# Kernel optimization log

Measured on AMD Instinct MI355X. Metric: run time of the kernel, lower is better.

The kernel has to match this reference:

```python
import jax, jax.numpy as jnp
import numpy as np

B, S, E, H = 2, 2048, 1024, 16
HD = E // H
CLAMP = 5.0


def setup_inputs() -> dict:
    key = jax.random.key(0)
    k1, k2, k3, k4 = jax.random.split(key, 4)
    # xavier-uniform-ish scale for weights
    lim_qkv = float(np.sqrt(6.0 / (E + 3 * E)))
    lim_o = float(np.sqrt(6.0 / (E + E)))
    return {
        "x": jax.random.normal(k1, (B, S, E), dtype=jnp.float32),
        "attn_bias": jax.random.normal(k2, (B, H, S, S), dtype=jnp.float32),
        "Wqkv": jax.random.uniform(k3, (3 * E, E), dtype=jnp.float32, minval=-lim_qkv, maxval=lim_qkv),
        "bqkv": jnp.zeros((3 * E,), dtype=jnp.float32),
        "Wo": jax.random.uniform(k4, (E, E), dtype=jnp.float32, minval=-lim_o, maxval=lim_o),
        "bo": jnp.zeros((E,), dtype=jnp.float32),
    }


def reference(x, attn_bias, Wqkv, bqkv, Wo, bo):
    b, s, e = x.shape
    # QKV projection: [B,S,3E] -> [B,S,H,3*HD] -> [B,H,S,3*HD]
    qkv = jnp.einsum("bse,fe->bsf", x, Wqkv) + bqkv
    qkv = qkv.reshape(b, s, H, 3 * HD).transpose(0, 2, 1, 3)
    q, k, v = jnp.split(qkv, 3, axis=-1)  # each [B,H,S,HD]
    # logits: bias added BEFORE 1/sqrt(d_k) scaling (as in source)
    logits = jnp.einsum("bhqd,bhkd->bhqk", q, k)
    logits = (logits + attn_bias) / jnp.sqrt(jnp.float32(HD))
    logits = jnp.clip(logits, -CLAMP, CLAMP)
    attn = jax.nn.softmax(logits, axis=-1)
    vals = jnp.einsum("bhqk,bhkd->bhqd", attn, v)
    vals = vals.transpose(0, 2, 1, 3).reshape(b, s, e)
    return jnp.einsum("bse,fe->bsf", vals, Wo) + bo
```

## Files before the change

kernel.cpp:

```cpp
#include <hip/hip_runtime.h>
#include <hip/hip_bf16.h>

#define NB 2
#define NS 2048
#define NE 1024
#define NH 16
#define HD 64

typedef __hip_bfloat16 bf16;
typedef __attribute__((ext_vector_type(8))) short bf16x8;
typedef __attribute__((ext_vector_type(4))) float f32x4;

typedef __attribute__((address_space(3))) void* lds_p;
typedef const __attribute__((address_space(1))) void* glb_p;

#define MFMA16(a, b, c) __builtin_amdgcn_mfma_f32_16x16x32_bf16((a), (b), (c), 0, 0, 0)

__device__ __forceinline__ void gl_lds16(const void* g, void* l) {
    __builtin_amdgcn_global_load_lds((glb_p)g, (lds_p)l, 16, 0, 0);
}

__device__ __forceinline__ bf16x8 ldv8(const bf16* p) { return *(const bf16x8*)p; }

__global__ __launch_bounds__(256) void cast3_k(const float* __restrict__ x,
                                               const float* __restrict__ wqkv,
                                               const float* __restrict__ wo,
                                               bf16* __restrict__ xb,
                                               bf16* __restrict__ wqkvb,
                                               bf16* __restrict__ wob) {
    const int n_x = NB * NS * NE / 4;
    const int n_q = 3 * NE * NE / 4;
    const int n_o = NE * NE / 4;
    int i = blockIdx.x * 256 + threadIdx.x;
    const float* in;
    bf16* out;
    int j;
    if (i < n_x) {
        in = x; out = xb; j = i;
    } else if (i < n_x + n_q) {
        in = wqkv; out = wqkvb; j = i - n_x;
    } else if (i < n_x + n_q + n_o) {
        in = wo; out = wob; j = i - n_x - n_q;
    } else {
        return;
    }
    float4 v = ((const float4*)in)[j];
    union { ushort4 u; bf16 b[4]; } pk;
    pk.b[0] = __float2bfloat16(v.x);
    pk.b[1] = __float2bfloat16(v.y);
    pk.b[2] = __float2bfloat16(v.z);
    pk.b[3] = __float2bfloat16(v.w);
    ((ushort4*)out)[j] = pk.u;
}

__global__ __launch_bounds__(256) void qkv_gemm(const bf16* __restrict__ A,
                                                const bf16* __restrict__ Bm,
                                                const float* __restrict__ bqkv,
                                                bf16* __restrict__ Qb, bf16* __restrict__ Kb,
                                                bf16* __restrict__ Vtb) {
    __shared__ bf16 As[128 * 32];
    __shared__ bf16 Bs[128 * 32];
    const int brow = blockIdx.x * 128;
    const int bcol = blockIdx.y * 128;
    const int t = threadIdx.x;
    const int w = t >> 6, lane = t & 63;
    const int wr = (w >> 1) * 64, wc = (w & 1) * 64;
    const int lr = lane & 15, lh = lane >> 4;
    const int K = 1024;

    f32x4 acc[4][4];
#pragma unroll
    for (int m = 0; m < 4; ++m)
#pragma unroll
        for (int n = 0; n < 4; ++n) acc[m][n] = (f32x4){0.f, 0.f, 0.f, 0.f};

    const bf16* ga0 = A + (size_t)(brow + (t >> 2)) * K + (t & 3) * 8;
    const bf16* ga1 = A + (size_t)(brow + 64 + (t >> 2)) * K + (t & 3) * 8;
    const bf16* gb0 = Bm + (size_t)(bcol + (t >> 2)) * K + (t & 3) * 8;
    const bf16* gb1 = Bm + (size_t)(bcol + 64 + (t >> 2)) * K + (t & 3) * 8;
    bf16* la0 = As + t * 8;
    bf16* la1 = As + 2048 + t * 8;
    bf16* lb0 = Bs + t * 8;
    bf16* lb1 = Bs + 2048 + t * 8;

    for (int kt = 0; kt < K; kt += 32) {
        gl_lds16(ga0 + kt, la0);
        gl_lds16(ga1 + kt, la1);
        gl_lds16(gb0 + kt, lb0);
        gl_lds16(gb1 + kt, lb1);
        __syncthreads();
        bf16x8 af[4], bfv[4];
#pragma unroll
        for (int m = 0; m < 4; ++m) af[m] = ldv8(&As[(wr + m * 16 + lr) * 32 + lh * 8]);
#pragma unroll
        for (int n = 0; n < 4; ++n) bfv[n] = ldv8(&Bs[(wc + n * 16 + lr) * 32 + lh * 8]);
#pragma unroll
        for (int m = 0; m < 4; ++m)
#pragma unroll
            for (int n = 0; n < 4; ++n) acc[m][n] = MFMA16(af[m], bfv[n], acc[m][n]);
        __syncthreads();
    }

#pragma unroll
    for (int n = 0; n < 4; ++n) {
        const int col = bcol + wc + n * 16 + lr;
        const int h = col / 192;
        const int r = col - h * 192;
        const int wh = r >> 6;
        const int d = r & 63;
        const float bq = bqkv[col];
#pragma unroll
        for (int m = 0; m < 4; ++m) {
            const int row0 = brow + wr + m * 16 + lh * 4;
            const int b = row0 >> 11;
            const int s0 = row0 & 2047;
            const size_t hb = (size_t)(b * NH + h) * (NS * HD);
            if (wh == 2) {
                alignas(8) bf16 tmp[4];
#pragma unroll
                for (int i = 0; i < 4; ++i) tmp[i] = __float2bfloat16(acc[m][n][i] + bq);
                *(ushort4*)(Vtb + hb + (size_t)d * NS + s0) = *(const ushort4*)tmp;
            } else {
                bf16* dst = (wh == 0 ? Qb : Kb) + hb + (size_t)s0 * HD + d;
#pragma unroll
                for (int i = 0; i < 4; ++i) dst[(size_t)i * HD] = __float2bfloat16(acc[m][n][i] + bq);
            }
        }
    }
}

__global__ __launch_bounds__(256, 4) void attn_k(const bf16* __restrict__ Qb,
                                                 const bf16* __restrict__ Kb,
                                                 const bf16* __restrict__ Vtb,
                                                 const float* __restrict__ bias,
                                                 bf16* __restrict__ valsb) {
    const int L = blockIdx.x;
    const int xcd = L & 7, kk = L >> 3;
    const int bh = (xcd << 2) | (kk >> 5);
    const int q0 = (kk & 31) * 64;
    const int t = threadIdx.x;
    const int w = t >> 6, lane = t & 63;
    const int lr = lane & 15, lh = lane >> 4;

    __shared__ bf16 Kls[2][64 * 64];
    __shared__ bf16 Vls[2][64 * 64];
    __shared__ bf16 Ps[4][16 * 64];

    const bf16* Qp = Qb + (size_t)bh * NS * HD;
    const bf16* Kp = Kb + (size_t)bh * NS * HD;
    const bf16* Vp = Vtb + (size_t)bh * HD * NS;

    const int qw = q0 + w * 16;
    bf16x8 qf0 = ldv8(&Qp[(qw + lr) * HD + lh * 8]);
    bf16x8 qf1 = ldv8(&Qp[(qw + lr) * HD + 32 + lh * 8]);

    const float* Bp = bias + (size_t)bh * NS * NS + (size_t)(qw + lr) * NS + lh * 4;

    const int srow0 = t >> 3;
    const int sce0 = ((t & 7) * 8) ^ ((srow0 & 7) << 3);
    const int srow1 = srow0 + 32;
    const int sce1 = ((t & 7) * 8) ^ ((srow1 & 7) << 3);

    f32x4 acc_o[4];
    float rowsum = 0.f;
#pragma unroll
    for (int n = 0; n < 4; ++n) acc_o[n] = (f32x4){0.f, 0.f, 0.f, 0.f};

    const float C1 = 0.18033688011112042f;
    const float C2 = 7.2134752044448170f;

    const int rswz = (lr & 7) << 3;
    const int ce0 = (lh * 8) ^ rswz;
    const int ce1 = (32 + lh * 8) ^ rswz;
    const int pswz = (lr & 7) << 3;

    gl_lds16(Kp + (size_t)srow0 * HD + sce0, &Kls[0][t * 8]);
    gl_lds16(Kp + (size_t)srow1 * HD + sce1, &Kls[0][2048 + t * 8]);
    gl_lds16(Vp + (size_t)srow0 * NS + sce0, &Vls[0][t * 8]);
    gl_lds16(Vp + (size_t)srow1 * NS + sce1, &Vls[0][2048 + t * 8]);
    __builtin_amdgcn_sched_barrier(0);
    float4 bvA[4], bvB[4];
#pragma unroll
    for (int n = 0; n < 4; ++n) bvA[n] = *(const float4*)(Bp + n * 16);
    __builtin_amdgcn_sched_barrier(0);
#pragma unroll
    for (int n = 0; n < 4; ++n) bvB[n] = *(const float4*)(Bp + 64 + n * 16);
    __builtin_amdgcn_sched_barrier(0);
    asm volatile("s_waitcnt vmcnt(8)" ::: "memory");
    __builtin_amdgcn_sched_barrier(0);
    __builtin_amdgcn_s_barrier();
    __builtin_amdgcn_sched_barrier(0);

#define ATTN_COMPUTE(CUR, BV)                                                         \
    {                                                                                 \
        const bf16* Kc = &Kls[CUR][0];                                                \
        f32x4 s[4];                                                                   \
        _Pragma("unroll") for (int n = 0; n < 4; ++n) {                               \
            bf16x8 k0 = ldv8(&Kc[(n * 16 + lr) * 64 + ce0]);                          \
            bf16x8 k1 = ldv8(&Kc[(n * 16 + lr) * 64 + ce1]);                          \
            s[n] = (f32x4){0.f, 0.f, 0.f, 0.f};                                       \
            s[n] = MFMA16(k0, qf0, s[n]);                                             \
            s[n] = MFMA16(k1, qf1, s[n]);                                             \
        }                                                                             \
        _Pragma("unroll") for (int n = 0; n < 4; ++n) {                               \
            union { ushort4 u; bf16 b[4]; } pk;                                       \
            _Pragma("unroll") for (int i = 0; i < 4; ++i) {                           \
                float bb = (i == 0   ? BV[n].x                                        \
                            : i == 1 ? BV[n].y                                        \
                            : i == 2 ? BV[n].z                                        \
                                     : BV[n].w);                                      \
                float xv = (s[n][i] + bb) * C1;                                       \
                xv = fminf(fmaxf(xv, -C2), C2);                                       \
                float p = exp2f(xv);                                                  \
                rowsum += p;                                                          \
                pk.b[i] = __float2bfloat16(p);                                        \
            }                                                                         \
            *(ushort4*)&Ps[w][lr * 64 + ((n * 16 + lh * 4) ^ pswz)] = pk.u;           \
        }                                                                             \
        bf16x8 pa0 = ldv8(&Ps[w][lr * 64 + ((lh * 8) ^ pswz)]);                       \
        bf16x8 pa1 = ldv8(&Ps[w][lr * 64 + (((32 + lh * 8)) ^ pswz)]);                \
        const bf16* Vc = &Vls[CUR][0];                                                \
        _Pragma("unroll") for (int n = 0; n < 4; ++n) {                               \
            bf16x8 v0 = ldv8(&Vc[(n * 16 + lr) * 64 + ce0]);                          \
            bf16x8 v1 = ldv8(&Vc[(n * 16 + lr) * 64 + ce1]);                          \
            acc_o[n] = MFMA16(pa0, v0, acc_o[n]);                                     \
            acc_o[n] = MFMA16(pa1, v1, acc_o[n]);                                     \
        }                                                                             \
    }

#define TILESTEP(CUR, BV, KTN)                                                        \
    {                                                                                 \
        bf16* Kd = &Kls[(CUR) ^ 1][0];                                                \
        bf16* Vd = &Vls[(CUR) ^ 1][0];                                                \
        gl_lds16(Kp + (size_t)((KTN) + srow0) * HD + sce0, Kd + t * 8);               \
        gl_lds16(Kp + (size_t)((KTN) + srow1) * HD + sce1, Kd + 2048 + t * 8);        \
        gl_lds16(Vp + (size_t)srow0 * NS + (KTN) + sce0, Vd + t * 8);                 \
        gl_lds16(Vp + (size_t)srow1 * NS + (KTN) + sce1, Vd + 2048 + t * 8);          \
        __builtin_amdgcn_sched_barrier(0);                                            \
        ATTN_COMPUTE(CUR, BV)                                                         \
        __builtin_amdgcn_sched_barrier(0);                                            \
        _Pragma("unroll") for (int n = 0; n < 4; ++n)                                 \
            BV[n] = *(const float4*)(Bp + (KTN) + 64 + n * 16);                       \
        __builtin_amdgcn_sched_barrier(0);                                            \
        asm volatile("s_waitcnt vmcnt(4)" ::: "memory");                              \
        __builtin_amdgcn_sched_barrier(0);                                            \
        __builtin_amdgcn_s_barrier();                                                 \
        __builtin_amdgcn_sched_barrier(0);                                            \
    }

    for (int it = 0; it < 15; ++it) {
        const int tt = it * 2;
        TILESTEP(0, bvA, (tt + 1) * 64)
        TILESTEP(1, bvB, (tt + 2) * 64)
    }

    {
        const int ktn = 31 * 64;
        bf16* Kd = &Kls[1][0];
        bf16* Vd = &Vls[1][0];
        gl_lds16(Kp + (size_t)(ktn + srow0) * HD + sce0, Kd + t * 8);
        gl_lds16(Kp + (size_t)(ktn + srow1) * HD + sce1, Kd + 2048 + t * 8);
        gl_lds16(Vp + (size_t)srow0 * NS + ktn + sce0, Vd + t * 8);
        gl_lds16(Vp + (size_t)srow1 * NS + ktn + sce1, Vd + 2048 + t * 8);
        __builtin_amdgcn_sched_barrier(0);
        ATTN_COMPUTE(0, bvA)
        __builtin_amdgcn_sched_barrier(0);
        asm volatile("s_waitcnt vmcnt(0)" ::: "memory");
        __builtin_amdgcn_sched_barrier(0);
        __builtin_amdgcn_s_barrier();
        __builtin_amdgcn_sched_barrier(0);
    }
    ATTN_COMPUTE(1, bvB)
#undef TILESTEP
#undef ATTN_COMPUTE

    rowsum += __shfl_xor(rowsum, 16, 64);
    rowsum += __shfl_xor(rowsum, 32, 64);
    float inv[4];
#pragma unroll
    for (int i = 0; i < 4; ++i) inv[i] = 1.0f / __shfl(rowsum, lh * 4 + i, 64);

    const int b = bh >> 4, h = bh & 15;
#pragma unroll
    for (int n = 0; n < 4; ++n) {
#pragma unroll
        for (int i = 0; i < 4; ++i) {
            const int qrow = qw + lh * 4 + i;
            valsb[(size_t)(b * NS + qrow) * NE + h * HD + n * 16 + lr] =
                __float2bfloat16(acc_o[n][i] * inv[i]);
        }
    }
}

__global__ __launch_bounds__(256) void out_gemm(const bf16* __restrict__ A,
                                                const bf16* __restrict__ Bm,
                                                const float* __restrict__ bo,
                                                float* __restrict__ out) {
    __shared__ bf16 As[128 * 32];
    __shared__ bf16 Bs[64 * 32];
    const int brow = blockIdx.x * 128;
    const int bcol = blockIdx.y * 64;
    const int t = threadIdx.x;
    const int w = t >> 6, lane = t & 63;
    const int wr = (w >> 1) * 64, wc = (w & 1) * 32;
    const int lr = lane & 15, lh = lane >> 4;
    const int K = 1024;

    f32x4 acc[4][2];
#pragma unroll
    for (int m = 0; m < 4; ++m)
#pragma unroll
        for (int n = 0; n < 2; ++n) acc[m][n] = (f32x4){0.f, 0.f, 0.f, 0.f};

    const bf16* ga0 = A + (size_t)(brow + (t >> 2)) * K + (t & 3) * 8;
    const bf16* ga1 = A + (size_t)(brow + 64 + (t >> 2)) * K + (t & 3) * 8;
    const bf16* gb0 = Bm + (size_t)(bcol + (t >> 2)) * K + (t & 3) * 8;
    bf16* la0 = As + t * 8;
    bf16* la1 = As + 2048 + t * 8;
    bf16* lb0 = Bs + t * 8;

    for (int kt = 0; kt < K; kt += 32) {
        gl_lds16(ga0 + kt, la0);
        gl_lds16(ga1 + kt, la1);
        gl_lds16(gb0 + kt, lb0);
        __syncthreads();
        bf16x8 af[4], bfv[2];
#pragma unroll
        for (int m = 0; m < 4; ++m) af[m] = ldv8(&As[(wr + m * 16 + lr) * 32 + lh * 8]);
#pragma unroll
        for (int n = 0; n < 2; ++n) bfv[n] = ldv8(&Bs[(wc + n * 16 + lr) * 32 + lh * 8]);
#pragma unroll
        for (int m = 0; m < 4; ++m)
#pragma unroll
            for (int n = 0; n < 2; ++n) acc[m][n] = MFMA16(af[m], bfv[n], acc[m][n]);
        __syncthreads();
    }

#pragma unroll
    for (int n = 0; n < 2; ++n) {
        const int col = bcol + wc + n * 16 + lr;
        const float bv = bo[col];
#pragma unroll
        for (int m = 0; m < 4; ++m) {
            const int row0 = brow + wr + m * 16 + lh * 4;
#pragma unroll
            for (int i = 0; i < 4; ++i) out[(size_t)(row0 + i) * NE + col] = acc[m][n][i] + bv;
        }
    }
}

extern "C" void kernel_launch(void* const* d_in, const int* in_sizes, int n_in,
                              void* d_out, int out_size, void* d_ws, size_t ws_size,
                              hipStream_t stream) {
    const float* x = (const float*)d_in[0];
    const float* attn_bias = (const float*)d_in[1];
    const float* Wqkv = (const float*)d_in[2];
    const float* bqkv = (const float*)d_in[3];
    const float* Wo = (const float*)d_in[4];
    const float* bo = (const float*)d_in[5];
    float* out = (float*)d_out;

    char* ws = (char*)d_ws;
    bf16* xb = (bf16*)(ws);
    bf16* Wqkvb = (bf16*)(ws + (8u << 20));
    bf16* Wob = (bf16*)(ws + (14u << 20));
    bf16* Qb = (bf16*)(ws + (16u << 20));
    bf16* Kb = (bf16*)(ws + (24u << 20));
    bf16* Vtb = (bf16*)(ws + (32u << 20));
    bf16* valsb = (bf16*)(ws + (40u << 20));

    cast3_k<<<8192, 256, 0, stream>>>(x, Wqkv, Wo, xb, Wqkvb, Wob);

    qkv_gemm<<<dim3(32, 24), 256, 0, stream>>>(xb, Wqkvb, bqkv, Qb, Kb, Vtb);

    attn_k<<<dim3(1024), 256, 0, stream>>>(Qb, Kb, Vtb, attn_bias, valsb);

    out_gemm<<<dim3(32, 16), 256, 0, stream>>>(valsb, Wob, bo, out);
}
```

Measured before the change: 212.0 us.

## Double-buffer GEMM LDS tiles, XCD-aware block mapping, prefetch bias earlier in attention

Both GEMMs now use two LDS buffers, so the next K-tile's global-to-LDS load is issued before the current tile is computed. The QKV GEMM also flattens its grid and remaps block indices so that blocks landing on the same XCD share column tiles, aiming for better L2 reuse of weights. The attention loop adds a third bias register set and issues the bias load for the next tile before the compute instead of after it, to hide global latency. This costs more LDS and registers, and the double-buffered GEMM loop has no wait on the async LDS loads before the barrier, which may be a correctness risk.

After: 230.1 us. 8.5% more time.

```diff
diff --git a/kernel.cpp b/kernel.cpp
--- a/kernel.cpp
+++ b/kernel.cpp
@@ -58,10 +58,12 @@
                                                 const float* __restrict__ bqkv,
                                                 bf16* __restrict__ Qb, bf16* __restrict__ Kb,
                                                 bf16* __restrict__ Vtb) {
-    __shared__ bf16 As[128 * 32];
-    __shared__ bf16 Bs[128 * 32];
-    const int brow = blockIdx.x * 128;
-    const int bcol = blockIdx.y * 128;
+    __shared__ bf16 As[2][128 * 32];
+    __shared__ bf16 Bs[2][128 * 32];
+    const int L = blockIdx.x;
+    const int xcd = L & 7, j = L >> 3;
+    const int bcol = (xcd * 3 + j % 3) * 128;
+    const int brow = (j / 3) * 128;
     const int t = threadIdx.x;
     const int w = t >> 6, lane = t & 63;
     const int wr = (w >> 1) * 64, wc = (w & 1) * 64;
@@ -78,28 +80,34 @@
     const bf16* ga1 = A + (size_t)(brow + 64 + (t >> 2)) * K + (t & 3) * 8;
     const bf16* gb0 = Bm + (size_t)(bcol + (t >> 2)) * K + (t & 3) * 8;
     const bf16* gb1 = Bm + (size_t)(bcol + 64 + (t >> 2)) * K + (t & 3) * 8;
-    bf16* la0 = As + t * 8;
-    bf16* la1 = As + 2048 + t * 8;
-    bf16* lb0 = Bs + t * 8;
-    bf16* lb1 = Bs + 2048 + t * 8;
-
-    for (int kt = 0; kt < K; kt += 32) {
-        gl_lds16(ga0 + kt, la0);
-        gl_lds16(ga1 + kt, la1);
-        gl_lds16(gb0 + kt, lb0);
-        gl_lds16(gb1 + kt, lb1);
-        __syncthreads();
+
+#define QKV_STAGE(S, B)                                                   \
+    {                                                                     \
+        gl_lds16(ga0 + (S) * 32, &As[B][0] + t * 8);                      \
+        gl_lds16(ga1 + (S) * 32, &As[B][2048] + t * 8);                   \
+        gl_lds16(gb0 + (S) * 32, &Bs[B][0] + t * 8);                      \
+        gl_lds16(gb1 + (S) * 32, &Bs[B][2048] + t * 8);                   \
+    }
+
+    QKV_STAGE(0, 0)
+    __syncthreads();
+
+    for (int tt = 0; tt < 32; ++tt) {
+        if (tt + 1 < 32) QKV_STAGE(tt + 1, (tt + 1) & 1)
+        const bf16* Ab = &As[tt & 1][0];
+        const bf16* Bb = &Bs[tt & 1][0];
         bf16x8 af[4], bfv[4];
 #pragma unroll
-        for (int m = 0; m < 4; ++m) af[m] = ldv8(&As[(wr + m * 16 + lr) * 32 + lh * 8]);
-#pragma unroll
-        for (int n = 0; n < 4; ++n) bfv[n] = ldv8(&Bs[(wc + n * 16 + lr) * 32 + lh * 8]);
+        for (int m = 0; m < 4; ++m) af[m] = ldv8(&Ab[(wr + m * 16 + lr) * 32 + lh * 8]);
+#pragma unroll
+        for (int n = 0; n < 4; ++n) bfv[n] = ldv8(&Bb[(wc + n * 16 + lr) * 32 + lh * 8]);
 #pragma unroll
         for (int m = 0; m < 4; ++m)
 #pragma unroll
             for (int n = 0; n < 4; ++n) acc[m][n] = MFMA16(af[m], bfv[n], acc[m][n]);
         __syncthreads();
     }
+#undef QKV_STAGE
 
 #pragma unroll
     for (int n = 0; n < 4; ++n) {
@@ -179,7 +187,7 @@
     gl_lds16(Vp + (size_t)srow0 * NS + sce0, &Vls[0][t * 8]);
     gl_lds16(Vp + (size_t)srow1 * NS + sce1, &Vls[0][2048 + t * 8]);
     __builtin_amdgcn_sched_barrier(0);
-    float4 bvA[4], bvB[4];
+    float4 bvA[4], bvB[4], bvC[4];
 #pragma unroll
     for (int n = 0; n < 4; ++n) bvA[n] = *(const float4*)(Bp + n * 16);
     __builtin_amdgcn_sched_barrier(0);
@@ -228,7 +236,7 @@
         }                                                                             \
     }
 
-#define TILESTEP(CUR, BV, KTN)                                                        \
+#define TILESTEP3(CUR, BVC, BVF, KTN)                                                 \
     {                                                                                 \
         bf16* Kd = &Kls[(CUR) ^ 1][0];                                                \
         bf16* Vd = &Vls[(CUR) ^ 1][0];                                                \
@@ -237,10 +245,10 @@
         gl_lds16(Vp + (size_t)srow0 * NS + (KTN) + sce0, Vd + t * 8);                 \
         gl_lds16(Vp + (size_t)srow1 * NS + (KTN) + sce1, Vd + 2048 + t * 8);          \
         __builtin_amdgcn_sched_barrier(0);                                            \
-        ATTN_COMPUTE(CUR, BV)                                                         \
-        __builtin_amdgcn_sched_barrier(0);                                            \
         _Pragma("unroll") for (int n = 0; n < 4; ++n)                                 \
-            BV[n] = *(const float4*)(Bp + (KTN) + 64 + n * 16);                       \
+            BVF[n] = *(const float4*)(Bp + (KTN) + 64 + n * 16);                      \
+        __builtin_amdgcn_sched_barrier(0);                                            \
+        ATTN_COMPUTE(CUR, BVC)                                                        \
         __builtin_amdgcn_sched_barrier(0);                                            \
         asm volatile("s_waitcnt vmcnt(4)" ::: "memory");                              \
         __builtin_amdgcn_sched_barrier(0);                                            \
@@ -248,10 +256,14 @@
         __builtin_amdgcn_sched_barrier(0);                                            \
     }
 
-    for (int it = 0; it < 15; ++it) {
-        const int tt = it * 2;
-        TILESTEP(0, bvA, (tt + 1) * 64)
-        TILESTEP(1, bvB, (tt + 2) * 64)
+    for (int it = 0; it < 5; ++it) {
+        const int tt = it * 6;
+        TILESTEP3(0, bvA, bvC, (tt + 1) * 64)
+        TILESTEP3(1, bvB, bvA, (tt + 2) * 64)
+        TILESTEP3(0, bvC, bvB, (tt + 3) * 64)
+        TILESTEP3(1, bvA, bvC, (tt + 4) * 64)
+        TILESTEP3(0, bvB, bvA, (tt + 5) * 64)
+        TILESTEP3(1, bvC, bvB, (tt + 6) * 64)
     }
 
     {
@@ -271,7 +283,7 @@
         __builtin_amdgcn_sched_barrier(0);
     }
     ATTN_COMPUTE(1, bvB)
-#undef TILESTEP
+#undef TILESTEP3
 #undef ATTN_COMPUTE
 
     rowsum += __shfl_xor(rowsum, 16, 64);
@@ -296,8 +308,8 @@
                                                 const bf16* __restrict__ Bm,
                                                 const float* __restrict__ bo,
                                                 float* __restrict__ out) {
-    __shared__ bf16 As[128 * 32];
-    __shared__ bf16 Bs[64 * 32];
+    __shared__ bf16 As[2][128 * 32];
+    __shared__ bf16 Bs[2][64 * 32];
     const int brow = blockIdx.x * 128;
     const int bcol = blockIdx.y * 64;
     const int t = threadIdx.x;
@@ -315,26 +327,33 @@
     const bf16* ga0 = A + (size_t)(brow + (t >> 2)) * K + (t & 3) * 8;
     const bf16* ga1 = A + (size_t)(brow + 64 + (t >> 2)) * K + (t & 3) * 8;
     const bf16* gb0 = Bm + (size_t)(bcol + (t >> 2)) * K + (t & 3) * 8;
-    bf16* la0 = As + t * 8;
-    bf16* la1 = As + 2048 + t * 8;
-    bf16* lb0 = Bs + t * 8;
-
-    for (int kt = 0; kt < K; kt += 32) {
-        gl_lds16(ga0 + kt, la0);
-        gl_lds16(ga1 + kt, la1);
-        gl_lds16(gb0 + kt, lb0);
-        __syncthreads();
+
+#define OUT_STAGE(S, B)                                                   \
+    {                                                                     \
+        gl_lds16(ga0 + (S) * 32, &As[B][0] + t * 8);                      \
+        gl_lds16(ga1 + (S) * 32, &As[B][2048] + t * 8);                   \
+        gl_lds16(gb0 + (S) * 32, &Bs[B][0] + t * 8);                      \
+    }
+
+    OUT_STAGE(0, 0)
+    __syncthreads();
+
+    for (int tt = 0; tt < 32; ++tt) {
+        if (tt + 1 < 32) OUT_STAGE(tt + 1, (tt + 1) & 1)
+        const bf16* Ab = &As[tt & 1][0];
+        const bf16* Bb = &Bs[tt & 1][0];
         bf16x8 af[4], bfv[2];
 #pragma unroll
-        for (int m = 0; m < 4; ++m) af[m] = ldv8(&As[(wr + m * 16 + lr) * 32 + lh * 8]);
-#pragma unroll
-        for (int n = 0; n < 2; ++n) bfv[n] = ldv8(&Bs[(wc + n * 16 + lr) * 32 + lh * 8]);
+        for (int m = 0; m < 4; ++m) af[m] = ldv8(&Ab[(wr + m * 16 + lr) * 32 + lh * 8]);
+#pragma unroll
+        for (int n = 0; n < 2; ++n) bfv[n] = ldv8(&Bb[(wc + n * 16 + lr) * 32 + lh * 8]);
 #pragma unroll
         for (int m = 0; m < 4; ++m)
 #pragma unroll
             for (int n = 0; n < 2; ++n) acc[m][n] = MFMA16(af[m], bfv[n], acc[m][n]);
         __syncthreads();
     }
+#undef OUT_STAGE
 
 #pragma unroll
     for (int n = 0; n < 2; ++n) {
@@ -371,7 +390,7 @@
 
     cast3_k<<<8192, 256, 0, stream>>>(x, Wqkv, Wo, xb, Wqkvb, Wob);
 
-    qkv_gemm<<<dim3(32, 24), 256, 0, stream>>>(xb, Wqkvb, bqkv, Qb, Kb, Vtb);
+    qkv_gemm<<<dim3(768), 256, 0, stream>>>(xb, Wqkvb, bqkv, Qb, Kb, Vtb);
 
     attn_k<<<dim3(1024), 256, 0, stream>>>(Qb, Kb, Vtb, attn_bias, valsb);
 
```
